# Performance work log

Hardware: AMD Instinct MI355X
Metric: run time of the kernel (lower is better)

Reference implementation:

```python
import jax, jax.numpy as jnp
import numpy as np

# dims
B, T, HID = 2, 2048, 2048
HK, HV, DK, DV, KW = 16, 32, 128, 128, 4
KEY_DIM = HK * DK          # 2048
VAL_DIM = HV * DV          # 4096
CONV_DIM = 2 * KEY_DIM + VAL_DIM  # 8192
EPS = 1e-6


def setup_inputs() -> dict:
    key = jax.random.key(0)
    ks = jax.random.split(key, 10)
    s = 0.02
    return {
        "x": jax.random.normal(ks[0], (B, T, HID), jnp.float32),
        "input_pos": jnp.arange(T, dtype=jnp.int64),
        "W_qkv": jax.random.normal(ks[1], (CONV_DIM, HID), jnp.float32) * s,
        "W_z": jax.random.normal(ks[2], (VAL_DIM, HID), jnp.float32) * s,
        "W_b": jax.random.normal(ks[3], (HV, HID), jnp.float32) * s,
        "W_a": jax.random.normal(ks[4], (HV, HID), jnp.float32) * s,
        "conv_w": jax.random.normal(ks[5], (CONV_DIM, 1, KW), jnp.float32) * 0.2,
        "dt_bias": jnp.ones((HV,), jnp.float32),
        "A_log": jnp.log(jax.random.uniform(ks[6], (HV,), jnp.float32, 1e-3, 16.0)),
        "norm_weight": jnp.ones((DV,), jnp.float32),
        "W_out": jax.random.normal(ks[7], (HID, VAL_DIM), jnp.float32) * s,
    }


def _l2norm(t):
    n = jnp.sqrt(jnp.sum(t * t, axis=-1, keepdims=True))
    return t / jnp.maximum(n, 1e-12)


def _gdn_scan(q, k, v, g, beta):
    # per-batch: q,k [T,HV,DK], v [T,HV,DV], g,beta [T,HV]
    scale = DK ** -0.5
    def step(S, inp):  # S: [HV, DK, DV]
        qt, kt, vt, gt, bt = inp
        S = S * jnp.exp(gt)[:, None, None]
        kv = jnp.einsum('hk,hkv->hv', kt, S)
        S = S + jnp.einsum('hk,hv->hkv', kt, bt[:, None] * (vt - kv))
        o = jnp.einsum('hk,hkv->hv', qt * scale, S)
        return S, o
    S0 = jnp.zeros((HV, DK, DV), q.dtype)
    _, o = jax.lax.scan(step, S0, (q, k, v, g, beta))
    return o  # [T, HV, DV]


def reference(x, input_pos, W_qkv, W_z, W_b, W_a, conv_w, dt_bias, A_log, norm_weight, W_out):
    # conv_state / recurrent_state buffers start at zero (and input_pos[0]==0 resets them),
    # so the causal conv reduces to left-padded depthwise conv and the scan starts from S=0.
    mixed_qkv = jnp.einsum('bth,ch->btc', x, W_qkv)                    # [B,T,CONV_DIM]
    z = jnp.einsum('bth,vh->btv', x, W_z).reshape(B, T, HV, DV)
    beta = jax.nn.sigmoid(jnp.einsum('bth,nh->btn', x, W_b))           # [B,T,HV]
    a = jnp.einsum('bth,nh->btn', x, W_a)
    g = -jnp.exp(A_log) * jax.nn.softplus(a + dt_bias)                 # [B,T,HV]

    # causal depthwise conv1d over time
    xc = mixed_qkv.transpose(0, 2, 1)                                  # [B,C,T]
    yc = jax.lax.conv_general_dilated(
        xc, conv_w, window_strides=(1,), padding=[(KW - 1, 0)],
        dimension_numbers=('NCH', 'OIH', 'NCH'), feature_group_count=CONV_DIM)
    qkv = jax.nn.silu(yc).transpose(0, 2, 1)                           # [B,T,C]

    q = qkv[..., :KEY_DIM].reshape(B, T, HK, DK)
    k = qkv[..., KEY_DIM:2 * KEY_DIM].reshape(B, T, HK, DK)
    v = qkv[..., 2 * KEY_DIM:].reshape(B, T, HV, DV)
    q = _l2norm(q)
    k = _l2norm(k)
    rep = HV // HK
    q = jnp.repeat(q, rep, axis=2)                                     # [B,T,HV,DK]
    k = jnp.repeat(k, rep, axis=2)

    o = jax.vmap(_gdn_scan)(q, k, v, g, beta)                          # [B,T,HV,DV]

    # gated RMSNorm: RMSNorm(o) * weight * silu(z)
    of = o.astype(jnp.float32)
    normed = of * jax.lax.rsqrt(jnp.mean(of * of, axis=-1, keepdims=True) + EPS)
    out = (norm_weight * normed) * jax.nn.silu(z.astype(jnp.float32))
    out = out.reshape(B, T, VAL_DIM)
    return jnp.einsum('btv,hv->bth', out, W_out)
```

## Files before the change

### kernel.cpp

```cpp
#include <hip/hip_runtime.h>

#define BB 2
#define TT 2048
#define HID 2048
#define HK 16
#define HV 32
#define DK 128
#define DV 128
#define KW 4
#define KEY_DIM 2048
#define VAL_DIM 4096
#define CONV_DIM 8192
#define N1PAD 12544
#define M_ROWS 4096
#define CC 64

typedef __attribute__((ext_vector_type(8))) short short8;
typedef __attribute__((ext_vector_type(8))) unsigned short ushort8;
typedef __attribute__((ext_vector_type(4))) float f32x4;

__device__ __forceinline__ unsigned short f2bf(float f) {
  union { float f; unsigned int u; } v; v.f = f;
  unsigned int r = v.u + 0x7FFFu + ((v.u >> 16) & 1u);
  return (unsigned short)(r >> 16);
}
__device__ __forceinline__ float bf2f(unsigned short u) {
  union { unsigned int u; float f; } v; v.u = ((unsigned int)u) << 16; return v.f;
}

template <int CTRL>
__device__ __forceinline__ float dpp_add(float v) {
  union { float f; int i; } a, b;
  a.f = v;
  b.i = __builtin_amdgcn_update_dpp(0, a.i, CTRL, 0xf, 0xf, true);
  return a.f + b.f;
}
template <int CTRL>
__device__ __forceinline__ int dpp_mov(int v) {
  return __builtin_amdgcn_update_dpp(0, v, CTRL, 0xf, 0xf, true);
}
__device__ __forceinline__ float row16_sum(float v) {
  v = dpp_add<0xB1>(v); v = dpp_add<0x4E>(v);
  v = dpp_add<0x141>(v); v = dpp_add<0x140>(v);
  return v;
}
__device__ __forceinline__ float row8_sum(float v) {
  v = dpp_add<0xB1>(v); v = dpp_add<0x4E>(v); v = dpp_add<0x141>(v);
  return v;
}

__device__ __forceinline__ void gload_lds16(const unsigned short* g, unsigned short* l) {
  __builtin_amdgcn_global_load_lds((const __attribute__((address_space(1))) unsigned int*)g,
                                   (__attribute__((address_space(3))) unsigned int*)l,
                                   16, 0, 0);
}
__device__ __forceinline__ void gload_lds4(const float* g, unsigned short* l) {
  __builtin_amdgcn_global_load_lds((const __attribute__((address_space(1))) unsigned int*)g,
                                   (__attribute__((address_space(3))) unsigned int*)l,
                                   4, 0, 0);
}

__device__ __forceinline__ short8 ldswz8(const char* base, int row, int e16) {
  int L = (row << 8) + (e16 << 1);
  return *(const short8*)(base + (L ^ ((row & 7) << 4)));
}
__device__ __forceinline__ short8 ldswz7(const char* base, int row, int e16) {
  int L = (row << 7) + (e16 << 1);
  return *(const short8*)(base + (L ^ ((row & 7) << 4)));
}

__global__ void cvt_bf16(const float* __restrict__ in, unsigned short* __restrict__ out) {
  long i = ((long)blockIdx.x * 256 + threadIdx.x) * 4;
  float4 v = *(const float4*)&in[i];
  unsigned long long p = (unsigned long long)f2bf(v.x)
                       | ((unsigned long long)f2bf(v.y) << 16)
                       | ((unsigned long long)f2bf(v.z) << 32)
                       | ((unsigned long long)f2bf(v.w) << 48);
  *(unsigned long long*)&out[i] = p;
}

__global__ void build_wcat(const float* __restrict__ wqkv, const float* __restrict__ wz,
                           const float* __restrict__ wb, const float* __restrict__ wa,
                           unsigned short* __restrict__ wcat) {
  long idx = (long)blockIdx.x * 256 + threadIdx.x;
  long e = idx * 4;
  long r = e >> 11;
  int cc = (int)(e & 2047);
  unsigned long long p = 0ULL;
  if (r < 12352) {
    const float* src;
    if (r < 8192)       src = wqkv + r * 2048;
    else if (r < 12288) src = wz + (r - 8192) * 2048;
    else if (r < 12320) src = wb + (r - 12288) * 2048;
    else                src = wa + (r - 12320) * 2048;
    float4 v = *(const float4*)&src[cc];
    p = (unsigned long long)f2bf(v.x)
      | ((unsigned long long)f2bf(v.y) << 16)
      | ((unsigned long long)f2bf(v.z) << 32)
      | ((unsigned long long)f2bf(v.w) << 48);
  }
  *(unsigned long long*)&wcat[e] = p;
}

__device__ __forceinline__ void stage256(const unsigned short* __restrict__ G, long rb, int K,
                                         int kt, char* region, int r, int tid, int wid) {
  int i = r * 512 + tid;
  int row = i >> 3;
  int D = i << 4;
  int eb = (D ^ ((row & 7) << 4)) & 127;
  const unsigned short* src = G + (rb + row) * (long)K + kt * 64 + (eb >> 1);
  gload_lds16(src, (unsigned short*)region + r * 4096 + wid * 512);
}

__global__ __launch_bounds__(512, 2) void gemm256(const unsigned short* __restrict__ A,
                                                  const unsigned short* __restrict__ Bw,
                                                  unsigned short* __restrict__ Cout,
                                                  int N, int K) {
  extern __shared__ char gs[];
  const int tid = threadIdx.x, wid = tid >> 6, lane = tid & 63;
  const int lr = lane & 15, lq = lane >> 4;
  const long m0 = (long)blockIdx.y << 8;
  const long n0 = (long)blockIdx.x << 8;
  const int wr = wid >> 2, wc = wid & 3;
  const int nkt = K >> 6;

  f32x4 acc[8][4] = {};

#pragma unroll
  for (int r = 0; r < 4; ++r) {
    stage256(A, m0, K, 0, gs, r, tid, wid);
    stage256(Bw, n0, K, 0, gs + 32768, r, tid, wid);
  }
  asm volatile("s_waitcnt vmcnt(0)" ::: "memory");
  __syncthreads();

  for (int kt = 0; kt < nkt; ++kt) {
    char* cur = gs + ((kt & 1) << 16);
    char* nxt = gs + (((kt + 1) & 1) << 16);
    const char* cA = cur;
    const char* cB = cur + 32768;
    const bool pf = (kt + 1 < nkt);
    short8 bf[2][4];
#pragma unroll
    for (int p = 0; p < 4; ++p) {
      if (pf) {
        stage256(A, m0, K, kt + 1, nxt, p, tid, wid);
        stage256(Bw, n0, K, kt + 1, nxt + 32768, p, tid, wid);
      }
      if (p == 0) {
#pragma unroll
        for (int ks = 0; ks < 2; ++ks)
#pragma unroll
          for (int cf = 0; cf < 4; ++cf)
            bf[ks][cf] = ldswz7(cB, wc * 64 + cf * 16 + lr, ks * 32 + lq * 8);
      }
      short8 af[2][2];
#pragma unroll
      for (int ks = 0; ks < 2; ++ks)
#pragma unroll
        for (int rr = 0; rr < 2; ++rr)
          af[ks][rr] = ldswz7(cA, wr * 128 + (p * 2 + rr) * 16 + lr, ks * 32 + lq * 8);
      __builtin_amdgcn_s_setprio(1);
#pragma unroll
      for (int ks = 0; ks < 2; ++ks)
#pragma unroll
        for (int rr = 0; rr < 2; ++rr)
#pragma unroll
          for (int cf = 0; cf < 4; ++cf)
            acc[p * 2 + rr][cf] = __builtin_amdgcn_mfma_f32_16x16x32_bf16(
                af[ks][rr], bf[ks][cf], acc[p * 2 + rr][cf], 0, 0, 0);
      __builtin_amdgcn_s_setprio(0);
    }
    asm volatile("s_waitcnt vmcnt(0)" ::: "memory");
    __syncthreads();
  }

  const long rbase = m0 + wr * 128 + lq * 4;
  const long cbase = n0 + wc * 64 + lr;
#pragma unroll
  for (int rf = 0; rf < 8; ++rf)
#pragma unroll
    for (int cf = 0; cf < 4; ++cf)
#pragma unroll
      for (int j = 0; j < 4; ++j)
        Cout[(rbase + rf * 16 + j) * N + cbase + cf * 16] = f2bf(acc[rf][cf][j]);
}

__global__ __launch_bounds__(512, 2) void gemm128x256(const unsigned short* __restrict__ A,
                                                      const unsigned short* __restrict__ Bw,
                                                      float* __restrict__ Cout,
                                                      int N, int K) {
  extern __shared__ char gs[];
  const int tid = threadIdx.x, wid = tid >> 6, lane = tid & 63;
  const int lr = lane & 15, lq = lane >> 4;
  const long m0 = (long)blockIdx.y << 7;
  const long n0 = (long)blockIdx.x << 8;
  const int wr = wid >> 2, wc = wid & 3;
  const int nkt = K >> 6;

  f32x4 acc[4][4] = {};

#pragma unroll
  for (int r = 0; r < 2; ++r) stage256(A, m0, K, 0, gs, r, tid, wid);
#pragma unroll
  for (int r = 0; r < 4; ++r) stage256(Bw, n0, K, 0, gs + 16384, r, tid, wid);
  asm volatile("s_waitcnt vmcnt(0)" ::: "memory");
  __syncthreads();

  for (int kt = 0; kt < nkt; ++kt) {
    char* cur = gs + (kt & 1) * 49152;
    char* nxt = gs + ((kt + 1) & 1) * 49152;
    const char* cA = cur;
    const char* cB = cur + 16384;
    const bool pf = (kt + 1 < nkt);
    short8 bf[2][4];
#pragma unroll
    for (int p = 0; p < 4; ++p) {
      if (pf) {
        if (p < 2) stage256(A, m0, K, kt + 1, nxt, p, tid, wid);
        stage256(Bw, n0, K, kt + 1, nxt + 16384, p, tid, wid);
      }
      if (p == 0) {
#pragma unroll
        for (int ks = 0; ks < 2; ++ks)
#pragma unroll
          for (int cf = 0; cf < 4; ++cf)
            bf[ks][cf] = ldswz7(cB, wc * 64 + cf * 16 + lr, ks * 32 + lq * 8);
      }
      short8 af[2];
#pragma unroll
      for (int ks = 0; ks < 2; ++ks)
        af[ks] = ldswz7(cA, wr * 64 + p * 16 + lr, ks * 32 + lq * 8);
      __builtin_amdgcn_s_setprio(1);
#pragma unroll
      for (int ks = 0; ks < 2; ++ks)
#pragma unroll
        for (int cf = 0; cf < 4; ++cf)
          acc[p][cf] = __builtin_amdgcn_mfma_f32_16x16x32_bf16(
              af[ks], bf[ks][cf], acc[p][cf], 0, 0, 0);
      __builtin_amdgcn_s_setprio(0);
    }
    asm volatile("s_waitcnt vmcnt(0)" ::: "memory");
    __syncthreads();
  }

  const long rbase = m0 + wr * 64 + lq * 4;
  const long cbase = n0 + wc * 64 + lr;
#pragma unroll
  for (int rf = 0; rf < 4; ++rf)
#pragma unroll
    for (int cf = 0; cf < 4; ++cf)
#pragma unroll
      for (int j = 0; j < 4; ++j)
        Cout[(rbase + rf * 16 + j) * N + cbase + cf * 16] = acc[rf][cf][j];
}

__global__ __launch_bounds__(256) void conv_silu(const unsigned short* __restrict__ C1,
                                                 const float* __restrict__ convw,
                                                 unsigned short* __restrict__ qb,
                                                 unsigned short* __restrict__ kb,
                                                 unsigned short* __restrict__ vb) {
  const int bid = blockIdx.x;
  const int cb = bid & 3, tblk = (bid >> 2) & 63, b = bid >> 8;
  const int c0 = cb * 2048 + threadIdx.x * 8;
  float w0[8], w1[8], w2[8], w3[8];
#pragma unroll
  for (int j = 0; j < 8; ++j) {
    float4 wv = *(const float4*)&convw[(c0 + j) * 4];
    w0[j] = wv.x; w1[j] = wv.y; w2[j] = wv.z; w3[j] = wv.w;
  }
  const int t0 = tblk * 32;
  const long rowbase = ((long)b * TT) * N1PAD + c0;
  float x0[8], x1[8], x2[8];
#pragma unroll
  for (int j = 0; j < 8; ++j) { x0[j] = 0.f; x1[j] = 0.f; x2[j] = 0.f; }
  if (t0 >= 1) { ushort8 r = *(const ushort8*)&C1[rowbase + (long)(t0 - 1) * N1PAD];
#pragma unroll
    for (int j = 0; j < 8; ++j) x2[j] = bf2f(r[j]); }
  if (t0 >= 2) { ushort8 r = *(const ushort8*)&C1[rowbase + (long)(t0 - 2) * N1PAD];
#pragma unroll
    for (int j = 0; j < 8; ++j) x1[j] = bf2f(r[j]); }
  if (t0 >= 3) { ushort8 r = *(const ushort8*)&C1[rowbase + (long)(t0 - 3) * N1PAD];
#pragma unroll
    for (int j = 0; j < 8; ++j) x0[j] = bf2f(r[j]); }

  const float nsc = (cb == 0) ? 0.08838834764831845f : 1.0f;
  for (int t = t0; t < t0 + 32; ++t) {
    ushort8 rr = *(const ushort8*)&C1[rowbase + (long)t * N1PAD];
    float ys[8];
#pragma unroll
    for (int j = 0; j < 8; ++j) {
      float x3 = bf2f(rr[j]);
      float y = w0[j] * x0[j] + w1[j] * x1[j] + w2[j] * x2[j] + w3[j] * x3;
      ys[j] = y / (1.f + __expf(-y));
      x0[j] = x1[j]; x1[j] = x2[j]; x2[j] = x3;
    }
    if (cb < 2) {
      float ss = 0.f;
#pragma unroll
      for (int j = 0; j < 8; ++j) ss = fmaf(ys[j], ys[j], ss);
      ss = row16_sum(ss);
      float sc = nsc / fmaxf(sqrtf(ss), 1e-12f);
#pragma unroll
      for (int j = 0; j < 8; ++j) ys[j] *= sc;
    }
    ushort8 outp;
#pragma unroll
    for (int j = 0; j < 8; ++j) outp[j] = f2bf(ys[j]);
    long m = (long)b * TT + t;
    if (cb == 0)      *(ushort8*)&qb[m * 2048 + threadIdx.x * 8] = outp;
    else if (cb == 1) *(ushort8*)&kb[m * 2048 + threadIdx.x * 8] = outp;
    else              *(ushort8*)&vb[m * 4096 + (cb - 2) * 2048 + threadIdx.x * 8] = outp;
  }
}

__global__ void gbeta(const unsigned short* __restrict__ C1, const float* __restrict__ Alog,
                      const float* __restrict__ dtb, float* __restrict__ graw, float* __restrict__ betab) {
  int idx = blockIdx.x * 256 + threadIdx.x;
  int m = idx >> 5, h = idx & 31;
  float a = bf2f(C1[(long)m * N1PAD + 12320 + h]);
  float bl = bf2f(C1[(long)m * N1PAD + 12288 + h]);
  float xsp = a + dtb[h];
  float sp = (xsp > 20.f) ? xsp : log1pf(expf(xsp));
  graw[idx] = -expf(Alog[h]) * sp;
  betab[idx] = 1.f / (1.f + expf(-bl));
}

#define OFF_K   0
#define OFF_V   16384
#define OFF_G   20480
#define OFF_B2  20736
#define OFF_KT  20992
#define OFF_SH  37376
#define OFF_SL  45568
#define OFF_A2  53760
#define OFF_MM  71168
#define OFF_BT  79360
#define OFF_BT2 83456
#define OFF_X   87552
#define OFF_CS  96000
#define OFF_EXC 96256
#define OFF_ECT 96512
#define SMEM_SZ 96768

__global__ __launch_bounds__(512, 2) void chunk_scan(const unsigned short* __restrict__ qb,
                                                     const unsigned short* __restrict__ kb,
                                                     const unsigned short* __restrict__ vb,
                                                     const float* __restrict__ graw,
                                                     const float* __restrict__ betab,
                                                     unsigned short* __restrict__ ob) {
  extern __shared__ char smem[];
  const int w = blockIdx.x;
  const int rdec = w >> 5, gdec = w & 31;
  const int bat = gdec >> 4, hk = gdec & 15;
  const int h = hk * 2 + (rdec >> 2), vc = rdec & 3;
  const int tid = threadIdx.x, wid = tid >> 6, lane = tid & 63;
  const int lr = lane & 15, lq = lane >> 4;
  const int rg = wid & 3, half = wid >> 2;
  const int mr = wid & 1, nc2 = (wid >> 1) & 3;

  const long kqoff = ((long)bat * TT) * 2048 + hk * 128;
  const long voff  = ((long)bat * TT) * 4096 + h * 128 + vc * 32;
  const long goff  = ((long)bat * TT) * 32 + h;

  f32x4 Smast[2] = {};

  auto stage_full = [&](int t0c) {
#pragma unroll
    for (int it = 0; it < 2; ++it) {
      int i = it * 512 + tid;
      int row = i >> 4;
      int L = ((i & 15) << 4) ^ ((row & 7) << 4);
      long grow = (long)(t0c + row) * 2048 + (L >> 1);
      gload_lds16(kb + kqoff + grow, (unsigned short*)(smem + OFF_K) + it * 4096 + wid * 512);
    }
    if (tid < 256)
      gload_lds16(vb + voff + (long)(t0c + (tid >> 2)) * 4096 + (tid & 3) * 8,
                  (unsigned short*)(smem + OFF_V) + wid * 512);
    if (wid == 6) gload_lds4(graw  + goff + (long)(t0c + lane) * 32, (unsigned short*)(smem + OFF_G));
    if (wid == 7) gload_lds4(betab + goff + (long)(t0c + lane) * 32, (unsigned short*)(smem + OFF_B2));
  };
  auto stage_part = [&](int t0c) {
    int tid2 = tid - 256, wid2 = wid - 4;
#pragma unroll
    for (int it = 0; it < 4; ++it) {
      int i = it * 256 + tid2;
      int row = i >> 4;
      int L = ((i & 15) << 4) ^ ((row & 7) << 4);
      long grow = (long)(t0c + row) * 2048 + (L >> 1);
      gload_lds16(kb + kqoff + grow, (unsigned short*)(smem + OFF_K) + it * 2048 + wid2 * 512);
    }
    gload_lds16(vb + voff + (long)(t0c + (tid2 >> 2)) * 4096 + (tid2 & 3) * 8,
                (unsigned short*)(smem + OFF_V) + wid2 * 512);
    if (wid == 4) gload_lds4(graw  + goff + (long)(t0c + lane) * 32, (unsigned short*)(smem + OFF_G));
    if (wid == 5) gload_lds4(betab + goff + (long)(t0c + lane) * 32, (unsigned short*)(smem + OFF_B2));
  };
  auto loadQ = [&](short8 (&qr)[4], int t0c) {
#pragma unroll
    for (int kk = 0; kk < 4; ++kk)
      qr[kk] = *(const short8*)&qb[kqoff + (long)(t0c + 16 * rg + lr) * 2048 + kk * 32 + lq * 8];
  };

  auto body = [&](int ct, short8 (&qcur)[4], short8 (&qnext)[4]) {
    {
      int tp = tid & 31, dkb = tid >> 5;
      short8 r0 = ldswz8(smem + OFF_K, 2 * tp, dkb * 8);
      short8 r1 = ldswz8(smem + OFF_K, 2 * tp + 1, dkb * 8);
#pragma unroll
      for (int e = 0; e < 8; ++e) {
        int dk = dkb * 8 + e;
        unsigned int pk = (unsigned int)(unsigned short)r0[e]
                        | ((unsigned int)(unsigned short)r1[e] << 16);
        int Lk = (dk << 7) + (tp << 2);
        *(unsigned int*)(smem + OFF_KT + (Lk ^ ((dk & 7) << 4))) = pk;
      }
    }
    if (wid == 0) {
      float gv = ((const float*)(smem + OFF_G))[lane];
#pragma unroll
      for (int off = 1; off < 64; off <<= 1) {
        float n = __shfl_up(gv, off);
        if (lane >= off) gv += n;
      }
      ((float*)(smem + OFF_CS))[lane] = gv;
      ((float*)(smem + OFF_EXC))[lane] = __expf(gv);
      float tot = __shfl(gv, 63);
      ((float*)(smem + OFF_ECT))[lane] = __expf(tot - gv);
    }
    __syncthreads();

    f32x4 aKK[2] = {}, aQK[2] = {}, aKS = {}, aQS = {};
    float oq[4];
#pragma unroll
    for (int kk = 0; kk < 4; ++kk) {
      int ke = kk * 32 + lq * 8;
      short8 avk = ldswz8(smem + OFF_K, 16 * rg + lr, ke);
      short8 avq = qcur[kk];
#pragma unroll
      for (int tc2 = 0; tc2 < 2; ++tc2) {
        short8 bvk = ldswz8(smem + OFF_K, 16 * (2 * half + tc2) + lr, ke);
        aKK[tc2] = __builtin_amdgcn_mfma_f32_16x16x32_bf16(avk, bvk, aKK[tc2], 0, 0, 0);
        aQK[tc2] = __builtin_amdgcn_mfma_f32_16x16x32_bf16(avq, bvk, aQK[tc2], 0, 0, 0);
      }
      short8 bH = ldswz8(smem + OFF_SH, 16 * half + lr, ke);
      short8 bL = ldswz8(smem + OFF_SL, 16 * half + lr, ke);
      aKS = __builtin_amdgcn_mfma_f32_16x16x32_bf16(avk, bH, aKS, 0, 0, 0);
      aKS = __builtin_amdgcn_mfma_f32_16x16x32_bf16(avk, bL, aKS, 0, 0, 0);
      aQS = __builtin_amdgcn_mfma_f32_16x16x32_bf16(avq, bH, aQS, 0, 0, 0);
      aQS = __builtin_amdgcn_mfma_f32_16x16x32_bf16(avq, bL, aQS, 0, 0, 0);
    }
    {
      const float* csp  = (const float*)(smem + OFF_CS);
      const float* excp = (const float*)(smem + OFF_EXC);
      const float* betp = (const float*)(smem + OFF_B2);
      const unsigned short* vp = (const unsigned short*)(smem + OFF_V);
      float cst[4], bt4[4], ext[4];
#pragma unroll
      for (int j = 0; j < 4; ++j) {
        int t = 16 * rg + lq * 4 + j;
        cst[j] = csp[t]; bt4[j] = betp[t]; ext[j] = excp[t];
      }
#pragma unroll
      for (int tc2 = 0; tc2 < 2; ++tc2) {
        int i = 16 * (2 * half + tc2) + lr;
        float csi = csp[i];
#pragma unroll
        for (int j = 0; j < 4; ++j) {
          int t = 16 * rg + lq * 4 + j;
          float e = __expf(cst[j] - csi);
          float av = (i < t) ? bt4[j] * e * aKK[tc2][j] : 0.f;
          ((float*)(smem + OFF_A2))[t * 68 + (i & 7) * 8 + (i >> 3)] = av;
          float mv = (i <= t) ? e * aQK[tc2][j] : 0.f;
          unsigned int mvb = f2bf(mv);
          unsigned int mvp = (unsigned int)dpp_mov<0xB1>((int)mvb);
          if (!(lr & 1)) {
            int Lm = (t << 7) + (i << 1);
            *(unsigned int*)(smem + OFF_MM + (Lm ^ ((t & 7) << 4))) = mvb | (mvp << 16);
          }
        }
      }
      int vcl = 16 * half + lr;
#pragma unroll
      for (int j = 0; j < 4; ++j) {
        int t = 16 * rg + lq * 4 + j;
        float vvv = bf2f(vp[t * 32 + vcl]);
        float x = bt4[j] * (vvv - ext[j] * aKS[j]);
        ((float*)(smem + OFF_X))[t * 33 + vcl] = x;
        oq[j] = ext[j] * aQS[j];
      }
    }
    __syncthreads();

    if (ct + 1 < TT / CC) loadQ(qnext, (ct + 1) * CC);
    if (wid < 4) {
      const float* A2p  = (const float*)(smem + OFF_A2);
      const float* Xp   = (const float*)(smem + OFF_X);
      const float* ectp = (const float*)(smem + OFF_ECT);
      const int col = tid >> 3, rr = tid & 7;
      float bbvX[8];
#pragma unroll
      for (int k = 0; k < 8; ++k) bbvX[k] = Xp[(8 * k + rr) * 33 + col];
      float bbv[8] = {0.f, 0.f, 0.f, 0.f, 0.f, 0.f, 0.f, 0.f};
#pragma unroll
      for (int t = 0; t < 64; ++t) {
        float4 a0 = *(const float4*)(A2p + t * 68 + rr * 8);
        float4 a1 = *(const float4*)(A2p + t * 68 + rr * 8 + 4);
        float sA = fmaf(a0.y, bbv[1], a0.x * bbv[0]);
        sA = fmaf(a0.z, bbv[2], sA); sA = fmaf(a0.w, bbv[3], sA);
        float sB = fmaf(a1.y, bbv[5], a1.x * bbv[4]);
        sB = fmaf(a1.z, bbv[6], sB); sB = fmaf(a1.w, bbv[7], sB);
        float s = row8_sum(sA + sB);
        float btv = bbvX[t >> 3] - s;
        if (rr == (t & 7)) bbv[t >> 3] = btv;
      }
#pragma unroll
      for (int k = 0; k < 8; ++k) {
        int t = 8 * k + rr;
        int Lb = (col << 7) + (t << 1);
        int Pb = Lb ^ ((col & 7) << 4);
        *(unsigned short*)(smem + OFF_BT + Pb)  = f2bf(bbv[k]);
        *(unsigned short*)(smem + OFF_BT2 + Pb) = f2bf(bbv[k] * ectp[t]);
      }
    } else if (ct + 1 < TT / CC) {
      stage_part((ct + 1) * CC);
    }
    __syncthreads();

    {
      f32x4 accO = (f32x4){oq[0], oq[1], oq[2], oq[3]};
#pragma unroll
      for (int kk2 = 0; kk2 < 2; ++kk2) {
        int ke = kk2 * 32 + lq * 8;
        short8 aM = ldswz7(smem + OFF_MM, 16 * rg + lr, ke);
        short8 bB = ldswz7(smem + OFF_BT, 16 * half + lr, ke);
        accO = __builtin_amdgcn_mfma_f32_16x16x32_bf16(aM, bB, accO, 0, 0, 0);
      }
      int vcl = 16 * half + lr;
#pragma unroll
      for (int j = 0; j < 4; ++j) {
        int t = 16 * rg + lq * 4 + j;
        long tg = (long)(bat * TT + ct * CC + t);
        ob[(tg * 32 + h) * 128 + vc * 32 + vcl] = f2bf(accO[j]);
      }

      f32x4 accP[2] = {};
#pragma unroll
      for (int kk2 = 0; kk2 < 2; ++kk2) {
        int ke = kk2 * 32 + lq * 8;
        short8 aB2 = ldswz7(smem + OFF_BT2, 16 * mr + lr, ke);
#pragma unroll
        for (int c4 = 0; c4 < 2; ++c4) {
          short8 bK = ldswz7(smem + OFF_KT, 16 * (2 * nc2 + c4) + lr, ke);
          accP[c4] = __builtin_amdgcn_mfma_f32_16x16x32_bf16(aB2, bK, accP[c4], 0, 0, 0);
        }
      }
      float ecC = ((const float*)(smem + OFF_EXC))[63];
#pragma unroll
      for (int c4 = 0; c4 < 2; ++c4)
#pragma unroll
        for (int j = 0; j < 4; ++j) {
          float sv = fmaf(ecC, Smast[c4][j], accP[c4][j]);
          Smast[c4][j] = sv;
          int vcr = 16 * mr + lq * 4 + j;
          int dk  = 16 * (2 * nc2 + c4) + lr;
          unsigned int hi = f2bf(sv);
          unsigned int lo = f2bf(sv - bf2f((unsigned short)hi));
          unsigned int hip = (unsigned int)dpp_mov<0xB1>((int)hi);
          unsigned int lop = (unsigned int)dpp_mov<0xB1>((int)lo);
          if (!(lr & 1)) {
            int Ls = (vcr << 8) + (dk << 1);
            int Ps = Ls ^ ((vcr & 7) << 4);
            *(unsigned int*)(smem + OFF_SH + Ps) = hi | (hip << 16);
            *(unsigned int*)(smem + OFF_SL + Ps) = lo | (lop << 16);
          }
        }
    }
    asm volatile("s_waitcnt vmcnt(0)" ::: "memory");
    __syncthreads();
  };

  short8 qA[4], qB[4];
  loadQ(qA, 0);
  stage_full(0);
  *(f32x4*)(smem + OFF_SH + tid * 32)      = (f32x4){0.f, 0.f, 0.f, 0.f};
  *(f32x4*)(smem + OFF_SH + tid * 32 + 16) = (f32x4){0.f, 0.f, 0.f, 0.f};
  asm volatile("s_waitcnt vmcnt(0)" ::: "memory");
  __syncthreads();

  for (int cp = 0; cp < TT / CC / 2; ++cp) {
    body(2 * cp, qA, qB);
    body(2 * cp + 1, qB, qA);
  }
}

__global__ __launch_bounds__(256) void norm_silu(const unsigned short* __restrict__ ob,
                                                 const unsigned short* __restrict__ C1,
                                                 const float* __restrict__ nw,
                                                 unsigned short* __restrict__ nrm) {
  int unit = blockIdx.x * 4 + (threadIdx.x >> 6);
  int lane = threadIdx.x & 63;
  int m = unit >> 5, h = unit & 31;
  unsigned int uo = *(const unsigned int*)&ob[(long)unit * 128 + lane * 2];
  float o0 = bf2f((unsigned short)(uo & 0xffff));
  float o1 = bf2f((unsigned short)(uo >> 16));
  float ss = o0 * o0 + o1 * o1;
#pragma unroll
  for (int mm = 1; mm < 64; mm <<= 1) ss += __shfl_xor(ss, mm);
  float rs = rsqrtf(ss * (1.0f / 128.0f) + 1e-6f);
  unsigned int uz = *(const unsigned int*)&C1[(long)m * N1PAD + 8192 + h * 128 + lane * 2];
  float z0 = bf2f((unsigned short)(uz & 0xffff));
  float z1 = bf2f((unsigned short)(uz >> 16));
  float s0 = z0 / (1.f + expf(-z0));
  float s1 = z1 / (1.f + expf(-z1));
  float r0 = o0 * rs * nw[lane * 2] * s0;
  float r1 = o1 * rs * nw[lane * 2 + 1] * s1;
  unsigned int pk = (unsigned int)f2bf(r0) | ((unsigned int)f2bf(r1) << 16);
  *(unsigned int*)&nrm[(long)unit * 128 + lane * 2] = pk;
}

extern "C" void kernel_launch(void* const* d_in, const int* in_sizes, int n_in,
                              void* d_out, int out_size, void* d_ws, size_t ws_size,
                              hipStream_t stream) {
  const float* x    = (const float*)d_in[0];
  const float* Wqkv = (const float*)d_in[2];
  const float* Wz   = (const float*)d_in[3];
  const float* Wb   = (const float*)d_in[4];
  const float* Wa   = (const float*)d_in[5];
  const float* convw= (const float*)d_in[6];
  const float* dtb  = (const float*)d_in[7];
  const float* Alog = (const float*)d_in[8];
  const float* nw   = (const float*)d_in[9];
  const float* Wout = (const float*)d_in[10];
  float* out = (float*)d_out;

  char* ws = (char*)d_ws;
  const size_t OFF_C1    = 0;
  const size_t OFF_XB    = 102760448;
  const size_t OFF_WCAT  = 119537664;
  const size_t OFF_QB    = OFF_XB;
  const size_t OFF_KB    = 119537664;
  const size_t OFF_VB    = 136314880;
  const size_t OFF_EG    = 170917888;
  const size_t OFF_BE    = 171442176;
  const size_t OFF_OB    = 171966464;
  const size_t OFF_NRM   = OFF_QB;
  const size_t OFF_WOUTB = OFF_VB;

  unsigned short* C1    = (unsigned short*)(ws + OFF_C1);
  unsigned short* xb    = (unsigned short*)(ws + OFF_XB);
  unsigned short* wcat  = (unsigned short*)(ws + OFF_WCAT);
  unsigned short* qbuf  = (unsigned short*)(ws + OFF_QB);
  unsigned short* kbuf  = (unsigned short*)(ws + OFF_KB);
  unsigned short* vbuf  = (unsigned short*)(ws + OFF_VB);
  float*          egb   = (float*)(ws + OFF_EG);
  float*          betab = (float*)(ws + OFF_BE);
  unsigned short* obuf  = (unsigned short*)(ws + OFF_OB);
  unsigned short* nrm   = (unsigned short*)(ws + OFF_NRM);
  unsigned short* woutb = (unsigned short*)(ws + OFF_WOUTB);
  (void)ws_size; (void)in_sizes; (void)n_in; (void)out_size;

  static int smem_set = 0;
  if (!smem_set) {
    hipFuncSetAttribute(reinterpret_cast<const void*>(chunk_scan),
                        hipFuncAttributeMaxDynamicSharedMemorySize, SMEM_SZ);
    hipFuncSetAttribute(reinterpret_cast<const void*>(gemm256),
                        hipFuncAttributeMaxDynamicSharedMemorySize, 131072);
    hipFuncSetAttribute(reinterpret_cast<const void*>(gemm128x256),
                        hipFuncAttributeMaxDynamicSharedMemorySize, 98304);
    smem_set = 1;
  }

  cvt_bf16<<<8192, 256, 0, stream>>>(x, xb);
  build_wcat<<<25088, 256, 0, stream>>>(Wqkv, Wz, Wb, Wa, wcat);
  gemm256<<<dim3(N1PAD / 256, M_ROWS / 256), 512, 131072, stream>>>(xb, wcat, C1, N1PAD, 2048);
  conv_silu<<<512, 256, 0, stream>>>(C1, convw, qbuf, kbuf, vbuf);
  gbeta<<<512, 256, 0, stream>>>(C1, Alog, dtb, egb, betab);
  chunk_scan<<<256, 512, SMEM_SZ, stream>>>(qbuf, kbuf, vbuf, egb, betab, obuf);
  cvt_bf16<<<8192, 256, 0, stream>>>(Wout, woutb);
  norm_silu<<<32768, 256, 0, stream>>>(obuf, C1, nw, nrm);
  gemm128x256<<<dim3(2048 / 256, M_ROWS / 128), 512, 98304, stream>>>(nrm, woutb, out, 2048, 4096);
}
```

Before: 718.8 us.

## Split chunk scan value dimension into 16-wide slices across twice as many blocks

The chunked gated-delta scan now splits each head's value dimension into eight 16-column slices instead of four 32-column slices, which doubles the grid to 512 blocks and shrinks shared memory per block. Wave roles are reassigned: half the waves handle output and state-projection MFMAs while the other half update the state, and launch bounds now request four blocks per CU. The aim is more parallelism and occupancy for the latency-bound sequential scan. In exchange the K/Q staging, KK/QK MFMAs and the decay-matrix work are duplicated across twice as many blocks, and several waves sit idle in some phases.

```diff
diff --git a/kernel.cpp b/kernel.cpp
--- a/kernel.cpp
+++ b/kernel.cpp
@@ -328,22 +328,22 @@
 
 #define OFF_K   0
 #define OFF_V   16384
-#define OFF_G   20480
-#define OFF_B2  20736
-#define OFF_KT  20992
-#define OFF_SH  37376
-#define OFF_SL  45568
-#define OFF_A2  53760
-#define OFF_MM  71168
-#define OFF_BT  79360
-#define OFF_BT2 83456
-#define OFF_X   87552
-#define OFF_CS  96000
-#define OFF_EXC 96256
-#define OFF_ECT 96512
-#define SMEM_SZ 96768
-
-__global__ __launch_bounds__(512, 2) void chunk_scan(const unsigned short* __restrict__ qb,
+#define OFF_G   18432
+#define OFF_B2  18688
+#define OFF_KT  18944
+#define OFF_SH  35328
+#define OFF_SL  39424
+#define OFF_A2  43520
+#define OFF_MM  60928
+#define OFF_BT  69120
+#define OFF_BT2 71168
+#define OFF_X   73216
+#define OFF_CS  77568
+#define OFF_EXC 77824
+#define OFF_ECT 78080
+#define SMEM_SZ 78336
+
+__global__ __launch_bounds__(512, 4) void chunk_scan(const unsigned short* __restrict__ qb,
                                                      const unsigned short* __restrict__ kb,
                                                      const unsigned short* __restrict__ vb,
                                                      const float* __restrict__ graw,
@@ -353,14 +353,13 @@
   const int w = blockIdx.x;
   const int rdec = w >> 5, gdec = w & 31;
   const int bat = gdec >> 4, hk = gdec & 15;
-  const int h = hk * 2 + (rdec >> 2), vc = rdec & 3;
+  const int h = hk * 2 + (rdec >> 3), vc = rdec & 7;
   const int tid = threadIdx.x, wid = tid >> 6, lane = tid & 63;
   const int lr = lane & 15, lq = lane >> 4;
   const int rg = wid & 3, half = wid >> 2;
-  const int mr = wid & 1, nc2 = (wid >> 1) & 3;
 
   const long kqoff = ((long)bat * TT) * 2048 + hk * 128;
-  const long voff  = ((long)bat * TT) * 4096 + h * 128 + vc * 32;
+  const long voff  = ((long)bat * TT) * 4096 + h * 128 + vc * 16;
   const long goff  = ((long)bat * TT) * 32 + h;
 
   f32x4 Smast[2] = {};
@@ -374,8 +373,8 @@
       long grow = (long)(t0c + row) * 2048 + (L >> 1);
       gload_lds16(kb + kqoff + grow, (unsigned short*)(smem + OFF_K) + it * 4096 + wid * 512);
     }
-    if (tid < 256)
-      gload_lds16(vb + voff + (long)(t0c + (tid >> 2)) * 4096 + (tid & 3) * 8,
+    if (tid < 128)
+      gload_lds16(vb + voff + (long)(t0c + (tid >> 1)) * 4096 + (tid & 1) * 8,
                   (unsigned short*)(smem + OFF_V) + wid * 512);
     if (wid == 6) gload_lds4(graw  + goff + (long)(t0c + lane) * 32, (unsigned short*)(smem + OFF_G));
     if (wid == 7) gload_lds4(betab + goff + (long)(t0c + lane) * 32, (unsigned short*)(smem + OFF_B2));
@@ -390,10 +389,11 @@
       long grow = (long)(t0c + row) * 2048 + (L >> 1);
       gload_lds16(kb + kqoff + grow, (unsigned short*)(smem + OFF_K) + it * 2048 + wid2 * 512);
     }
-    gload_lds16(vb + voff + (long)(t0c + (tid2 >> 2)) * 4096 + (tid2 & 3) * 8,
-                (unsigned short*)(smem + OFF_V) + wid2 * 512);
-    if (wid == 4) gload_lds4(graw  + goff + (long)(t0c + lane) * 32, (unsigned short*)(smem + OFF_G));
-    if (wid == 5) gload_lds4(betab + goff + (long)(t0c + lane) * 32, (unsigned short*)(smem + OFF_B2));
+    if (tid2 < 128)
+      gload_lds16(vb + voff + (long)(t0c + (tid2 >> 1)) * 4096 + (tid2 & 1) * 8,
+                  (unsigned short*)(smem + OFF_V) + wid2 * 512);
+    if (wid == 6) gload_lds4(graw  + goff + (long)(t0c + lane) * 32, (unsigned short*)(smem + OFF_G));
+    if (wid == 7) gload_lds4(betab + goff + (long)(t0c + lane) * 32, (unsigned short*)(smem + OFF_B2));
   };
   auto loadQ = [&](short8 (&qr)[4], int t0c) {
 #pragma unroll
@@ -442,12 +442,14 @@
         aKK[tc2] = __builtin_amdgcn_mfma_f32_16x16x32_bf16(avk, bvk, aKK[tc2], 0, 0, 0);
         aQK[tc2] = __builtin_amdgcn_mfma_f32_16x16x32_bf16(avq, bvk, aQK[tc2], 0, 0, 0);
       }
-      short8 bH = ldswz8(smem + OFF_SH, 16 * half + lr, ke);
-      short8 bL = ldswz8(smem + OFF_SL, 16 * half + lr, ke);
-      aKS = __builtin_amdgcn_mfma_f32_16x16x32_bf16(avk, bH, aKS, 0, 0, 0);
-      aKS = __builtin_amdgcn_mfma_f32_16x16x32_bf16(avk, bL, aKS, 0, 0, 0);
-      aQS = __builtin_amdgcn_mfma_f32_16x16x32_bf16(avq, bH, aQS, 0, 0, 0);
-      aQS = __builtin_amdgcn_mfma_f32_16x16x32_bf16(avq, bL, aQS, 0, 0, 0);
+      if (half == 0) {
+        short8 bH = ldswz8(smem + OFF_SH, lr, ke);
+        short8 bL = ldswz8(smem + OFF_SL, lr, ke);
+        aKS = __builtin_amdgcn_mfma_f32_16x16x32_bf16(avk, bH, aKS, 0, 0, 0);
+        aKS = __builtin_amdgcn_mfma_f32_16x16x32_bf16(avk, bL, aKS, 0, 0, 0);
+        aQS = __builtin_amdgcn_mfma_f32_16x16x32_bf16(avq, bH, aQS, 0, 0, 0);
+        aQS = __builtin_amdgcn_mfma_f32_16x16x32_bf16(avq, bL, aQS, 0, 0, 0);
+      }
     }
     {
       const float* csp  = (const float*)(smem + OFF_CS);
@@ -479,27 +481,29 @@
           }
         }
       }
-      int vcl = 16 * half + lr;
-#pragma unroll
-      for (int j = 0; j < 4; ++j) {
-        int t = 16 * rg + lq * 4 + j;
-        float vvv = bf2f(vp[t * 32 + vcl]);
-        float x = bt4[j] * (vvv - ext[j] * aKS[j]);
-        ((float*)(smem + OFF_X))[t * 33 + vcl] = x;
-        oq[j] = ext[j] * aQS[j];
+      if (half == 0) {
+        int vcl = lr;
+#pragma unroll
+        for (int j = 0; j < 4; ++j) {
+          int t = 16 * rg + lq * 4 + j;
+          float vvv = bf2f(vp[t * 16 + vcl]);
+          float x = bt4[j] * (vvv - ext[j] * aKS[j]);
+          ((float*)(smem + OFF_X))[t * 17 + vcl] = x;
+          oq[j] = ext[j] * aQS[j];
+        }
       }
     }
     __syncthreads();
 
     if (ct + 1 < TT / CC) loadQ(qnext, (ct + 1) * CC);
-    if (wid < 4) {
+    if (wid < 2) {
       const float* A2p  = (const float*)(smem + OFF_A2);
       const float* Xp   = (const float*)(smem + OFF_X);
       const float* ectp = (const float*)(smem + OFF_ECT);
       const int col = tid >> 3, rr = tid & 7;
       float bbvX[8];
 #pragma unroll
-      for (int k = 0; k < 8; ++k) bbvX[k] = Xp[(8 * k + rr) * 33 + col];
+      for (int k = 0; k < 8; ++k) bbvX[k] = Xp[(8 * k + rr) * 17 + col];
       float bbv[8] = {0.f, 0.f, 0.f, 0.f, 0.f, 0.f, 0.f, 0.f};
 #pragma unroll
       for (int t = 0; t < 64; ++t) {
@@ -521,36 +525,37 @@
         *(unsigned short*)(smem + OFF_BT + Pb)  = f2bf(bbv[k]);
         *(unsigned short*)(smem + OFF_BT2 + Pb) = f2bf(bbv[k] * ectp[t]);
       }
-    } else if (ct + 1 < TT / CC) {
+    } else if (wid >= 4 && ct + 1 < TT / CC) {
       stage_part((ct + 1) * CC);
     }
     __syncthreads();
 
-    {
+    if (half == 0) {
       f32x4 accO = (f32x4){oq[0], oq[1], oq[2], oq[3]};
 #pragma unroll
       for (int kk2 = 0; kk2 < 2; ++kk2) {
         int ke = kk2 * 32 + lq * 8;
         short8 aM = ldswz7(smem + OFF_MM, 16 * rg + lr, ke);
-        short8 bB = ldswz7(smem + OFF_BT, 16 * half + lr, ke);
+        short8 bB = ldswz7(smem + OFF_BT, lr, ke);
         accO = __builtin_amdgcn_mfma_f32_16x16x32_bf16(aM, bB, accO, 0, 0, 0);
       }
-      int vcl = 16 * half + lr;
+      int vcl = lr;
 #pragma unroll
       for (int j = 0; j < 4; ++j) {
         int t = 16 * rg + lq * 4 + j;
         long tg = (long)(bat * TT + ct * CC + t);
-        ob[(tg * 32 + h) * 128 + vc * 32 + vcl] = f2bf(accO[j]);
-      }
-
+        ob[(tg * 32 + h) * 128 + vc * 16 + vcl] = f2bf(accO[j]);
+      }
+    } else {
+      int ws2 = wid - 4;
       f32x4 accP[2] = {};
 #pragma unroll
       for (int kk2 = 0; kk2 < 2; ++kk2) {
         int ke = kk2 * 32 + lq * 8;
-        short8 aB2 = ldswz7(smem + OFF_BT2, 16 * mr + lr, ke);
+        short8 aB2 = ldswz7(smem + OFF_BT2, lr, ke);
 #pragma unroll
         for (int c4 = 0; c4 < 2; ++c4) {
-          short8 bK = ldswz7(smem + OFF_KT, 16 * (2 * nc2 + c4) + lr, ke);
+          short8 bK = ldswz7(smem + OFF_KT, 16 * (2 * ws2 + c4) + lr, ke);
           accP[c4] = __builtin_amdgcn_mfma_f32_16x16x32_bf16(aB2, bK, accP[c4], 0, 0, 0);
         }
       }
@@ -561,8 +566,8 @@
         for (int j = 0; j < 4; ++j) {
           float sv = fmaf(ecC, Smast[c4][j], accP[c4][j]);
           Smast[c4][j] = sv;
-          int vcr = 16 * mr + lq * 4 + j;
-          int dk  = 16 * (2 * nc2 + c4) + lr;
+          int vcr = lq * 4 + j;
+          int dk  = 16 * (2 * ws2 + c4) + lr;
           unsigned int hi = f2bf(sv);
           unsigned int lo = f2bf(sv - bf2f((unsigned short)hi));
           unsigned int hip = (unsigned int)dpp_mov<0xB1>((int)hi);
@@ -582,8 +587,7 @@
   short8 qA[4], qB[4];
   loadQ(qA, 0);
   stage_full(0);
-  *(f32x4*)(smem + OFF_SH + tid * 32)      = (f32x4){0.f, 0.f, 0.f, 0.f};
-  *(f32x4*)(smem + OFF_SH + tid * 32 + 16) = (f32x4){0.f, 0.f, 0.f, 0.f};
+  *(f32x4*)(smem + OFF_SH + tid * 16) = (f32x4){0.f, 0.f, 0.f, 0.f};
   asm volatile("s_waitcnt vmcnt(0)" ::: "memory");
   __syncthreads();
 
@@ -675,7 +679,7 @@
   gemm256<<<dim3(N1PAD / 256, M_ROWS / 256), 512, 131072, stream>>>(xb, wcat, C1, N1PAD, 2048);
   conv_silu<<<512, 256, 0, stream>>>(C1, convw, qbuf, kbuf, vbuf);
   gbeta<<<512, 256, 0, stream>>>(C1, Alog, dtb, egb, betab);
-  chunk_scan<<<256, 512, SMEM_SZ, stream>>>(qbuf, kbuf, vbuf, egb, betab, obuf);
+  chunk_scan<<<512, 512, SMEM_SZ, stream>>>(qbuf, kbuf, vbuf, egb, betab, obuf);
   cvt_bf16<<<8192, 256, 0, stream>>>(Wout, woutb);
   norm_silu<<<32768, 256, 0, stream>>>(obuf, C1, nw, nrm);
   gemm128x256<<<dim3(2048 / 256, M_ROWS / 128), 512, 98304, stream>>>(nrm, woutb, out, 2048, 4096);
```

New measurement: 1.131 ms. +57.3%, slower.

## Double-buffer K transpose and gate cumsum to drop a barrier per chunk

Applied to the files above, without the earlier changes.

In the chunk scan, the K transpose and gate cumsum tables now go into double-buffered shared memory slots. They are computed for the next chunk at the tail of the current chunk, which removes the __syncthreads that used to sit at the start of each chunk body. In both GEMM kernels, all next-tile prefetch loads are issued up front instead of being spread across the MFMA phases, and the B fragment loads are hoisted out of the phase loop. The cost is about 17KB more LDS per block in chunk_scan, which may affect the 2-blocks-per-CU occupancy, plus a vmcnt wait moved earlier in the chunk.

```diff
diff --git a/kernel.cpp b/kernel.cpp
--- a/kernel.cpp
+++ b/kernel.cpp
@@ -14,6 +14,7 @@
 #define N1PAD 12544
 #define M_ROWS 4096
 #define CC 64
+#define NCH 32
 
 typedef __attribute__((ext_vector_type(8))) short short8;
 typedef __attribute__((ext_vector_type(8))) unsigned short ushort8;
@@ -139,21 +140,21 @@
     char* nxt = gs + (((kt + 1) & 1) << 16);
     const char* cA = cur;
     const char* cB = cur + 32768;
-    const bool pf = (kt + 1 < nkt);
+    if (kt + 1 < nkt) {
+#pragma unroll
+      for (int r = 0; r < 4; ++r) {
+        stage256(A, m0, K, kt + 1, nxt, r, tid, wid);
+        stage256(Bw, n0, K, kt + 1, nxt + 32768, r, tid, wid);
+      }
+    }
     short8 bf[2][4];
 #pragma unroll
+    for (int ks = 0; ks < 2; ++ks)
+#pragma unroll
+      for (int cf = 0; cf < 4; ++cf)
+        bf[ks][cf] = ldswz7(cB, wc * 64 + cf * 16 + lr, ks * 32 + lq * 8);
+#pragma unroll
     for (int p = 0; p < 4; ++p) {
-      if (pf) {
-        stage256(A, m0, K, kt + 1, nxt, p, tid, wid);
-        stage256(Bw, n0, K, kt + 1, nxt + 32768, p, tid, wid);
-      }
-      if (p == 0) {
-#pragma unroll
-        for (int ks = 0; ks < 2; ++ks)
-#pragma unroll
-          for (int cf = 0; cf < 4; ++cf)
-            bf[ks][cf] = ldswz7(cB, wc * 64 + cf * 16 + lr, ks * 32 + lq * 8);
-      }
       short8 af[2][2];
 #pragma unroll
       for (int ks = 0; ks < 2; ++ks)
@@ -212,21 +213,20 @@
     char* nxt = gs + ((kt + 1) & 1) * 49152;
     const char* cA = cur;
     const char* cB = cur + 16384;
-    const bool pf = (kt + 1 < nkt);
+    if (kt + 1 < nkt) {
+#pragma unroll
+      for (int r = 0; r < 2; ++r) stage256(A, m0, K, kt + 1, nxt, r, tid, wid);
+#pragma unroll
+      for (int r = 0; r < 4; ++r) stage256(Bw, n0, K, kt + 1, nxt + 16384, r, tid, wid);
+    }
     short8 bf[2][4];
 #pragma unroll
+    for (int ks = 0; ks < 2; ++ks)
+#pragma unroll
+      for (int cf = 0; cf < 4; ++cf)
+        bf[ks][cf] = ldswz7(cB, wc * 64 + cf * 16 + lr, ks * 32 + lq * 8);
+#pragma unroll
     for (int p = 0; p < 4; ++p) {
-      if (pf) {
-        if (p < 2) stage256(A, m0, K, kt + 1, nxt, p, tid, wid);
-        stage256(Bw, n0, K, kt + 1, nxt + 16384, p, tid, wid);
-      }
-      if (p == 0) {
-#pragma unroll
-        for (int ks = 0; ks < 2; ++ks)
-#pragma unroll
-          for (int cf = 0; cf < 4; ++cf)
-            bf[ks][cf] = ldswz7(cB, wc * 64 + cf * 16 + lr, ks * 32 + lq * 8);
-      }
       short8 af[2];
 #pragma unroll
       for (int ks = 0; ks < 2; ++ks)
@@ -331,17 +331,15 @@
 #define OFF_G   20480
 #define OFF_B2  20736
 #define OFF_KT  20992
-#define OFF_SH  37376
-#define OFF_SL  45568
-#define OFF_A2  53760
-#define OFF_MM  71168
-#define OFF_BT  79360
-#define OFF_BT2 83456
-#define OFF_X   87552
-#define OFF_CS  96000
-#define OFF_EXC 96256
-#define OFF_ECT 96512
-#define SMEM_SZ 96768
+#define OFF_SH  53760
+#define OFF_SL  61952
+#define OFF_A2  70144
+#define OFF_MM  87552
+#define OFF_BT  95744
+#define OFF_BT2 99840
+#define OFF_X   103936
+#define OFF_TBL 112384
+#define SMEM_SZ 113920
 
 __global__ __launch_bounds__(512, 2) void chunk_scan(const unsigned short* __restrict__ qb,
                                                      const unsigned short* __restrict__ kb,
@@ -401,20 +399,21 @@
       qr[kk] = *(const short8*)&qb[kqoff + (long)(t0c + 16 * rg + lr) * 2048 + kk * 32 + lq * 8];
   };
 
-  auto body = [&](int ct, short8 (&qcur)[4], short8 (&qnext)[4]) {
-    {
-      int tp = tid & 31, dkb = tid >> 5;
-      short8 r0 = ldswz8(smem + OFF_K, 2 * tp, dkb * 8);
-      short8 r1 = ldswz8(smem + OFF_K, 2 * tp + 1, dkb * 8);
-#pragma unroll
-      for (int e = 0; e < 8; ++e) {
-        int dk = dkb * 8 + e;
-        unsigned int pk = (unsigned int)(unsigned short)r0[e]
-                        | ((unsigned int)(unsigned short)r1[e] << 16);
-        int Lk = (dk << 7) + (tp << 2);
-        *(unsigned int*)(smem + OFF_KT + (Lk ^ ((dk & 7) << 4))) = pk;
-      }
-    }
+  auto transposeK = [&](int tb2) {
+    char* ktb = smem + OFF_KT + tb2 * 16384;
+    int tp = tid & 31, dkb = tid >> 5;
+    short8 r0 = ldswz8(smem + OFF_K, 2 * tp, dkb * 8);
+    short8 r1 = ldswz8(smem + OFF_K, 2 * tp + 1, dkb * 8);
+#pragma unroll
+    for (int e = 0; e < 8; ++e) {
+      int dk = dkb * 8 + e;
+      unsigned int pk = (unsigned int)(unsigned short)r0[e]
+                      | ((unsigned int)(unsigned short)r1[e] << 16);
+      int Lk = (dk << 7) + (tp << 2);
+      *(unsigned int*)(ktb + (Lk ^ ((dk & 7) << 4))) = pk;
+    }
+  };
+  auto cumsumG = [&](int tb2) {
     if (wid == 0) {
       float gv = ((const float*)(smem + OFF_G))[lane];
 #pragma unroll
@@ -422,12 +421,19 @@
         float n = __shfl_up(gv, off);
         if (lane >= off) gv += n;
       }
-      ((float*)(smem + OFF_CS))[lane] = gv;
-      ((float*)(smem + OFF_EXC))[lane] = __expf(gv);
+      float* T = (float*)(smem + OFF_TBL + tb2 * 768);
+      T[lane] = gv;
+      T[64 + lane] = __expf(gv);
       float tot = __shfl(gv, 63);
-      ((float*)(smem + OFF_ECT))[lane] = __expf(tot - gv);
-    }
-    __syncthreads();
+      T[128 + lane] = __expf(tot - gv);
+    }
+  };
+
+  auto body = [&](int ct, short8 (&qcur)[4], short8 (&qnext)[4]) {
+    const int tb = ct & 1;
+    const float* csp  = (const float*)(smem + OFF_TBL + tb * 768);
+    const float* excp = csp + 64;
+    const float* ectp = csp + 128;
 
     f32x4 aKK[2] = {}, aQK[2] = {}, aKS = {}, aQS = {};
     float oq[4];
@@ -450,8 +456,6 @@
       aQS = __builtin_amdgcn_mfma_f32_16x16x32_bf16(avq, bL, aQS, 0, 0, 0);
     }
     {
-      const float* csp  = (const float*)(smem + OFF_CS);
-      const float* excp = (const float*)(smem + OFF_EXC);
       const float* betp = (const float*)(smem + OFF_B2);
       const unsigned short* vp = (const unsigned short*)(smem + OFF_V);
       float cst[4], bt4[4], ext[4];
@@ -491,11 +495,10 @@
     }
     __syncthreads();
 
-    if (ct + 1 < TT / CC) loadQ(qnext, (ct + 1) * CC);
+    if (ct + 1 < NCH) loadQ(qnext, (ct + 1) * CC);
     if (wid < 4) {
-      const float* A2p  = (const float*)(smem + OFF_A2);
-      const float* Xp   = (const float*)(smem + OFF_X);
-      const float* ectp = (const float*)(smem + OFF_ECT);
+      const float* A2p = (const float*)(smem + OFF_A2);
+      const float* Xp  = (const float*)(smem + OFF_X);
       const int col = tid >> 3, rr = tid & 7;
       float bbvX[8];
 #pragma unroll
@@ -521,12 +524,14 @@
         *(unsigned short*)(smem + OFF_BT + Pb)  = f2bf(bbv[k]);
         *(unsigned short*)(smem + OFF_BT2 + Pb) = f2bf(bbv[k] * ectp[t]);
       }
-    } else if (ct + 1 < TT / CC) {
+    } else if (ct + 1 < NCH) {
       stage_part((ct + 1) * CC);
     }
+    asm volatile("s_waitcnt vmcnt(0)" ::: "memory");
     __syncthreads();
 
     {
+      const char* ktb = smem + OFF_KT + tb * 16384;
       f32x4 accO = (f32x4){oq[0], oq[1], oq[2], oq[3]};
 #pragma unroll
       for (int kk2 = 0; kk2 < 2; ++kk2) {
@@ -550,11 +555,11 @@
         short8 aB2 = ldswz7(smem + OFF_BT2, 16 * mr + lr, ke);
 #pragma unroll
         for (int c4 = 0; c4 < 2; ++c4) {
-          short8 bK = ldswz7(smem + OFF_KT, 16 * (2 * nc2 + c4) + lr, ke);
+          short8 bK = ldswz7(ktb, 16 * (2 * nc2 + c4) + lr, ke);
           accP[c4] = __builtin_amdgcn_mfma_f32_16x16x32_bf16(aB2, bK, accP[c4], 0, 0, 0);
         }
       }
-      float ecC = ((const float*)(smem + OFF_EXC))[63];
+      float ecC = excp[63];
 #pragma unroll
       for (int c4 = 0; c4 < 2; ++c4)
 #pragma unroll
@@ -575,7 +580,10 @@
           }
         }
     }
-    asm volatile("s_waitcnt vmcnt(0)" ::: "memory");
+    if (ct + 1 < NCH) {
+      transposeK(tb ^ 1);
+      cumsumG(tb ^ 1);
+    }
     __syncthreads();
   };
 
@@ -586,8 +594,11 @@
   *(f32x4*)(smem + OFF_SH + tid * 32 + 16) = (f32x4){0.f, 0.f, 0.f, 0.f};
   asm volatile("s_waitcnt vmcnt(0)" ::: "memory");
   __syncthreads();
-
-  for (int cp = 0; cp < TT / CC / 2; ++cp) {
+  transposeK(0);
+  cumsumG(0);
+  __syncthreads();
+
+  for (int cp = 0; cp < NCH / 2; ++cp) {
     body(2 * cp, qA, qB);
     body(2 * cp + 1, qB, qA);
   }
```

After: 727.8 us. No clear change (+1.2%).

## Deepen gemm256 pipeline to four-stage ring with K-tile of 32

Applied to the files above, without the earlier changes.

Restructures the 256x256 GEMM main loop from a double-buffered 64-wide K tile into a 4-slot ring of 32-wide K tiles, prefetching three tiles ahead. It uses partial vmcnt waits and a raw s_barrier instead of full drains, so global loads overlap more compute. A new swizzle for 64-byte rows is added. The cost is more loop iterations and barriers per unit of K, with the same LDS footprint.

```diff
diff --git a/kernel.cpp b/kernel.cpp
--- a/kernel.cpp
+++ b/kernel.cpp
@@ -67,6 +67,10 @@
 __device__ __forceinline__ short8 ldswz7(const char* base, int row, int e16) {
   int L = (row << 7) + (e16 << 1);
   return *(const short8*)(base + (L ^ ((row & 7) << 4)));
+}
+__device__ __forceinline__ short8 ldswz6(const char* base, int row, int e16) {
+  int L = (row << 6) + (e16 << 1);
+  return *(const short8*)(base + (L ^ ((row & 3) << 4)));
 }
 
 __global__ void cvt_bf16(const float* __restrict__ in, unsigned short* __restrict__ out) {
@@ -111,6 +115,14 @@
   const unsigned short* src = G + (rb + row) * (long)K + kt * 64 + (eb >> 1);
   gload_lds16(src, (unsigned short*)region + r * 4096 + wid * 512);
 }
+__device__ __forceinline__ void stage32(const unsigned short* __restrict__ G, long rb, int K,
+                                        int kt, char* region, int r, int tid, int wid) {
+  int i = r * 512 + tid;
+  int row = i >> 2;
+  int eb = ((i & 3) << 4) ^ ((row & 3) << 4);
+  const unsigned short* src = G + (rb + row) * (long)K + kt * 32 + (eb >> 1);
+  gload_lds16(src, (unsigned short*)region + r * 4096 + wid * 512);
+}
 
 __global__ __launch_bounds__(512, 2) void gemm256(const unsigned short* __restrict__ A,
                                                   const unsigned short* __restrict__ Bw,
@@ -122,57 +134,52 @@
   const long m0 = (long)blockIdx.y << 8;
   const long n0 = (long)blockIdx.x << 8;
   const int wr = wid >> 2, wc = wid & 3;
-  const int nkt = K >> 6;
+  const int nkt = K >> 5;
 
   f32x4 acc[8][4] = {};
 
 #pragma unroll
-  for (int r = 0; r < 4; ++r) {
-    stage256(A, m0, K, 0, gs, r, tid, wid);
-    stage256(Bw, n0, K, 0, gs + 32768, r, tid, wid);
-  }
-  asm volatile("s_waitcnt vmcnt(0)" ::: "memory");
-  __syncthreads();
+  for (int t = 0; t < 3; ++t) {
+    char* nb = gs + t * 32768;
+#pragma unroll
+    for (int r = 0; r < 2; ++r) {
+      stage32(A, m0, K, t, nb, r, tid, wid);
+      stage32(Bw, n0, K, t, nb + 16384, r, tid, wid);
+    }
+  }
+  asm volatile("s_waitcnt vmcnt(8)" ::: "memory");
+  __builtin_amdgcn_s_barrier();
 
   for (int kt = 0; kt < nkt; ++kt) {
-    char* cur = gs + ((kt & 1) << 16);
-    char* nxt = gs + (((kt + 1) & 1) << 16);
+    const char* cur = gs + (kt & 3) * 32768;
     const char* cA = cur;
-    const char* cB = cur + 32768;
-    const bool pf = (kt + 1 < nkt);
-    short8 bf[2][4];
-#pragma unroll
-    for (int p = 0; p < 4; ++p) {
-      if (pf) {
-        stage256(A, m0, K, kt + 1, nxt, p, tid, wid);
-        stage256(Bw, n0, K, kt + 1, nxt + 32768, p, tid, wid);
-      }
-      if (p == 0) {
-#pragma unroll
-        for (int ks = 0; ks < 2; ++ks)
-#pragma unroll
-          for (int cf = 0; cf < 4; ++cf)
-            bf[ks][cf] = ldswz7(cB, wc * 64 + cf * 16 + lr, ks * 32 + lq * 8);
-      }
-      short8 af[2][2];
-#pragma unroll
-      for (int ks = 0; ks < 2; ++ks)
-#pragma unroll
-        for (int rr = 0; rr < 2; ++rr)
-          af[ks][rr] = ldswz7(cA, wr * 128 + (p * 2 + rr) * 16 + lr, ks * 32 + lq * 8);
-      __builtin_amdgcn_s_setprio(1);
-#pragma unroll
-      for (int ks = 0; ks < 2; ++ks)
-#pragma unroll
-        for (int rr = 0; rr < 2; ++rr)
-#pragma unroll
-          for (int cf = 0; cf < 4; ++cf)
-            acc[p * 2 + rr][cf] = __builtin_amdgcn_mfma_f32_16x16x32_bf16(
-                af[ks][rr], bf[ks][cf], acc[p * 2 + rr][cf], 0, 0, 0);
-      __builtin_amdgcn_s_setprio(0);
-    }
-    asm volatile("s_waitcnt vmcnt(0)" ::: "memory");
-    __syncthreads();
+    const char* cB = cur + 16384;
+    if (kt + 3 < nkt) {
+      char* nb = gs + ((kt + 3) & 3) * 32768;
+#pragma unroll
+      for (int r = 0; r < 2; ++r) {
+        stage32(A, m0, K, kt + 3, nb, r, tid, wid);
+        stage32(Bw, n0, K, kt + 3, nb + 16384, r, tid, wid);
+      }
+    }
+    short8 bf[4], af[8];
+#pragma unroll
+    for (int cf = 0; cf < 4; ++cf)
+      bf[cf] = ldswz6(cB, wc * 64 + cf * 16 + lr, lq * 8);
+#pragma unroll
+    for (int rf = 0; rf < 8; ++rf)
+      af[rf] = ldswz6(cA, wr * 128 + rf * 16 + lr, lq * 8);
+    __builtin_amdgcn_s_setprio(1);
+#pragma unroll
+    for (int rf = 0; rf < 8; ++rf)
+#pragma unroll
+      for (int cf = 0; cf < 4; ++cf)
+        acc[rf][cf] = __builtin_amdgcn_mfma_f32_16x16x32_bf16(af[rf], bf[cf], acc[rf][cf], 0, 0, 0);
+    __builtin_amdgcn_s_setprio(0);
+    if (kt + 3 < nkt)      asm volatile("s_waitcnt vmcnt(8)" ::: "memory");
+    else if (kt + 2 < nkt) asm volatile("s_waitcnt vmcnt(4)" ::: "memory");
+    else if (kt + 1 < nkt) asm volatile("s_waitcnt vmcnt(0)" ::: "memory");
+    __builtin_amdgcn_s_barrier();
   }
 
   const long rbase = m0 + wr * 128 + lq * 4;
```

Result: slower. 739.9 us (+2.9%).
